# Kernel tuning notes

Measured on AMD Instinct MI355X. Metric: run time of the kernel, lower is better.

The kernel has to match this reference:

```python
import jax, jax.numpy as jnp
import numpy as np

B, N, D_V, D_H, D_K = 1024, 131072, 256, 256, 256


def setup_inputs() -> dict:
    key = jax.random.key(0)
    ks = jax.random.split(key, 12)
    s = 0.02
    V = jax.random.normal(ks[0], (B, D_V), dtype=jnp.float32)
    H = jax.random.normal(ks[1], (N, D_H), dtype=jnp.float32)
    batch_idx = jnp.sort(jax.random.randint(ks[2], (N,), 0, B)).astype(jnp.int32)
    Wq = jax.random.normal(ks[3], (D_K, D_V), dtype=jnp.float32) / np.sqrt(D_V)
    bq = jnp.zeros((D_K,), dtype=jnp.float32)
    Wk = jax.random.normal(ks[4], (D_K, D_H), dtype=jnp.float32) / np.sqrt(D_H)
    bk = jnp.zeros((D_K,), dtype=jnp.float32)
    Wv = jax.random.normal(ks[5], (D_V, D_H), dtype=jnp.float32) / np.sqrt(D_H)
    bv = jnp.zeros((D_V,), dtype=jnp.float32)
    Wo = jax.random.normal(ks[6], (D_V, 2 * D_V), dtype=jnp.float32) / np.sqrt(2 * D_V)
    bo = jnp.zeros((D_V,), dtype=jnp.float32)
    return {"V": V, "H": H, "batch_idx": batch_idx,
            "Wq": Wq, "bq": bq, "Wk": Wk, "bk": bk,
            "Wv": Wv, "bv": bv, "Wo": Wo, "bo": bo}


def reference(V, H, batch_idx, Wq, bq, Wk, bk, Wv, bv, Wo, bo):
    nb = V.shape[0]
    Q = V @ Wq.T + bq            # [B, d_k] one query per graph
    K = H @ Wk.T + bk            # [N, d_k]
    Vval = H @ Wv.T + bv         # [N, d_v]
    scale = 1.0 / jnp.sqrt(jnp.asarray(K.shape[-1], K.dtype))
    # ragged attention scores: each node attends to its graph's query
    scores = jnp.einsum('nd,nd->n', K, Q[batch_idx]) * scale   # [N]
    m = jax.ops.segment_max(scores, batch_idx, num_segments=nb)  # [B]
    e = jnp.exp(scores - m[batch_idx])
    denom = jax.ops.segment_sum(e, batch_idx, num_segments=nb)   # [B]
    attn = e / denom[batch_idx]                                  # [N]
    H_tilde = jax.ops.segment_sum(attn[:, None] * Vval, batch_idx, num_segments=nb)  # [B, d_v]
    U = jnp.concatenate([V, H_tilde], axis=-1)                   # [B, 2*d_v]
    out = U @ Wo.T + bo                                          # [B, d_v]
    # graphs with zero nodes pass V through unchanged
    count = jax.ops.segment_sum(jnp.ones_like(scores), batch_idx, num_segments=nb)
    return jnp.where((count > 0)[:, None], out, V)
```

## Files before the change

### kernel.cpp

```cpp
#include <hip/hip_runtime.h>
#include <math.h>

#define D 256
#define TWOD 512
#define BB 1024
#define NN 131072
#define LOG2E 1.4426950408889634f

typedef float v4f __attribute__((ext_vector_type(4)));

__device__ __forceinline__ v4f ldg_nt(const float* p, bool valid) {
  v4f z = {0.f, 0.f, 0.f, 0.f};
  if (valid) z = __builtin_nontemporal_load((const v4f*)p);
  return z;
}

__device__ __forceinline__ float dot4(v4f a, v4f b) {
  return fmaf(a.w, b.w, fmaf(a.z, b.z, fmaf(a.y, b.y, a.x * b.x)));
}

__global__ __launch_bounds__(256) void prep_kernel(
    const float* __restrict__ Wq, const float* __restrict__ bq,
    const float* __restrict__ Wk, const float* __restrict__ Wv,
    const float* __restrict__ bv, const float* __restrict__ Wo,
    const float* __restrict__ bo, const int* __restrict__ bidx,
    float* __restrict__ Mt, float* __restrict__ WfT,
    float* __restrict__ bqt, float* __restrict__ cvec,
    int* __restrict__ offs) {
  const int blk = blockIdx.x;
  const int t = threadIdx.x;
  if (blk < 64) {
    const int d0 = blk * 4;
    float a0 = 0.f, a1 = 0.f, a2 = 0.f, a3 = 0.f;
    for (int e = 0; e < D; ++e) {
      const float wk = Wk[(size_t)e * D + t];
      const float* wqr = Wq + (size_t)e * D + d0;
      a0 = fmaf(wqr[0], wk, a0);
      a1 = fmaf(wqr[1], wk, a1);
      a2 = fmaf(wqr[2], wk, a2);
      a3 = fmaf(wqr[3], wk, a3);
    }
    Mt[(size_t)(d0 + 0) * D + t] = a0;
    Mt[(size_t)(d0 + 1) * D + t] = a1;
    Mt[(size_t)(d0 + 2) * D + t] = a2;
    Mt[(size_t)(d0 + 3) * D + t] = a3;
  } else if (blk < 128) {
    const int h0 = (blk - 64) * 4;
    float a0 = 0.f, a1 = 0.f, a2 = 0.f, a3 = 0.f;
    for (int v = 0; v < D; ++v) {
      const float wo = Wo[(size_t)t * TWOD + D + v];
      const float* wvr = Wv + (size_t)v * D + h0;
      a0 = fmaf(wvr[0], wo, a0);
      a1 = fmaf(wvr[1], wo, a1);
      a2 = fmaf(wvr[2], wo, a2);
      a3 = fmaf(wvr[3], wo, a3);
    }
    WfT[(size_t)(D + h0 + 0) * D + t] = a0;
    WfT[(size_t)(D + h0 + 1) * D + t] = a1;
    WfT[(size_t)(D + h0 + 2) * D + t] = a2;
    WfT[(size_t)(D + h0 + 3) * D + t] = a3;
  } else if (blk < 144) {
    __shared__ float tile[64][65];
    const int b = blk - 128;
    const int r0 = (b >> 2) * 64, c0 = (b & 3) * 64;
    const int lane = t & 63, sr = t >> 6;
    #pragma unroll 4
    for (int rr = 0; rr < 16; ++rr) {
      const int r = rr * 4 + sr;
      tile[r][lane] = Wo[(size_t)(r0 + r) * TWOD + c0 + lane];
    }
    __syncthreads();
    #pragma unroll 4
    for (int rr = 0; rr < 16; ++rr) {
      const int r = rr * 4 + sr;
      WfT[(size_t)(c0 + r) * D + r0 + lane] = tile[lane][r];
    }
  } else if (blk == 144) {
    float a = 0.f;
    for (int e = 0; e < D; ++e)
      a = fmaf(Wk[(size_t)e * D + t], bq[e], a);
    bqt[t] = a;
  } else if (blk == 145) {
    float a = bo[t];
    for (int v = 0; v < D; ++v)
      a = fmaf(Wo[(size_t)t * TWOD + D + v], bv[v], a);
    cvec[t] = a;
  } else {
    const int i = (blk - 146) * 256 + t;
    if (i >= NN) return;
    const int b1 = bidx[i];
    const int b2 = (i + 1 < NN) ? bidx[i + 1] : BB;
    if (i == 0) {
      for (int b = 0; b <= b1; ++b) offs[b] = 0;
    }
    for (int b = b1 + 1; b <= b2; ++b) offs[b] = i + 1;
  }
}

__global__ __launch_bounds__(1024) void f_kernel(
    const float* __restrict__ H, const float* __restrict__ V,
    const float* __restrict__ Mt, const float* __restrict__ bqt,
    const int* __restrict__ offs, const float* __restrict__ WfT,
    const float* __restrict__ cvec, float* __restrict__ out) {
  __shared__ __align__(16) char smem[32768 + 4096 + 8192];
  float (*partq)[4][D] = (float(*)[4][D])smem;
  float (*ss)[D] = (float(*)[D])smem;
  float (*part)[4][D] = (float(*)[4][D])smem;
  float* Vs  = (float*)(smem + 32768);
  float* Us2 = (float*)(smem + 36864);
  __shared__ float sm[16], sd[16];

  const int t = threadIdx.x;
  const int wave = t >> 6, lane = t & 63;
  const int blk = blockIdx.x;
  const int b0 = blk * 4;

  {
    const int i = t >> 8, d = t & 255;
    Vs[i * 256 + d] = V[(size_t)(b0 + i) * D + d];
  }
  __syncthreads();

  {
    v4f a0 = {0.f, 0.f, 0.f, 0.f}, a1 = a0, a2 = a0, a3 = a0;
    const int db = wave * 16;
    #pragma unroll 4
    for (int dd = 0; dd < 16; ++dd) {
      const int d = db + dd;
      const v4f w4 = *(const v4f*)(Mt + (size_t)d * D + lane * 4);
      a0 += w4 * Vs[0 * 256 + d];
      a1 += w4 * Vs[1 * 256 + d];
      a2 += w4 * Vs[2 * 256 + d];
      a3 += w4 * Vs[3 * 256 + d];
    }
    if (wave >= 8) {
      *(v4f*)&partq[wave - 8][0][lane * 4] = a0;
      *(v4f*)&partq[wave - 8][1][lane * 4] = a1;
      *(v4f*)&partq[wave - 8][2][lane * 4] = a2;
      *(v4f*)&partq[wave - 8][3][lane * 4] = a3;
    }
    __syncthreads();
    if (wave < 8) {
      v4f p0 = *(const v4f*)&partq[wave][0][lane * 4];
      v4f p1 = *(const v4f*)&partq[wave][1][lane * 4];
      v4f p2 = *(const v4f*)&partq[wave][2][lane * 4];
      v4f p3 = *(const v4f*)&partq[wave][3][lane * 4];
      *(v4f*)&partq[wave][0][lane * 4] = a0 + p0;
      *(v4f*)&partq[wave][1][lane * 4] = a1 + p1;
      *(v4f*)&partq[wave][2][lane * 4] = a2 + p2;
      *(v4f*)&partq[wave][3][lane * 4] = a3 + p3;
    }
  }
  __syncthreads();

  const int ib = wave >> 2, qq = wave & 3;
  const int bb = b0 + ib;
  const int start = offs[bb], end = offs[bb + 1];

  v4f q4 = *(const v4f*)(bqt + lane * 4);
  #pragma unroll
  for (int w = 0; w < 8; ++w) q4 += *(const v4f*)&partq[w][ib][lane * 4];
  __syncthreads();

  float m = -1e30f, den = 0.f;
  v4f acc = {0.f, 0.f, 0.f, 0.f};
  {
    const float SC = 0.0625f * LOG2E;
    const int odd = lane & 1;
    int n = start + qq * 2;
    v4f c0 = ldg_nt(H + (size_t)n * D + lane * 4, n < end);
    v4f c1 = ldg_nt(H + (size_t)(n + 1) * D + lane * 4, n + 1 < end);
    while (n < end) {
      const int nn = n + 8;
      v4f p0 = ldg_nt(H + (size_t)nn * D + lane * 4, nn < end);
      v4f p1 = ldg_nt(H + (size_t)(nn + 1) * D + lane * 4, nn + 1 < end);

      const float d0 = dot4(c0, q4);
      const float d1 = dot4(c1, q4);
      const float mine = odd ? d1 : d0;
      const float oth  = odd ? d0 : d1;
      float s = mine + __shfl_xor(oth, 1);
      s += __shfl_xor(s, 2);
      s += __shfl_xor(s, 4);
      s += __shfl_xor(s, 8);
      s += __shfl_xor(s, 16);
      s += __shfl_xor(s, 32);
      const float sc = (n + odd < end) ? s * SC : -1e30f;

      const float mm = fmaxf(sc, __shfl_xor(sc, 1));
      const float nm = fmaxf(m, mm);
      const float f = exp2f(m - nm);
      const float w = exp2f(sc - nm);
      const float wx = __shfl_xor(w, 1);
      const float wr0 = odd ? wx : w;
      const float wr1 = odd ? w : wx;
      den = fmaf(den, f, w + wx);
      acc = acc * f + c0 * wr0 + c1 * wr1;
      m = nm;

      c0 = p0; c1 = p1; n = nn;
    }
  }
  *(v4f*)&ss[wave][lane * 4] = acc;
  if (lane == 0) { sm[wave] = m; sd[wave] = den; }
  __syncthreads();

  {
    const int i = t >> 8, d = t & 255;
    const int w0 = i * 4;
    const float m0 = sm[w0], m1 = sm[w0 + 1], m2 = sm[w0 + 2], m3 = sm[w0 + 3];
    const float M = fmaxf(fmaxf(m0, m1), fmaxf(m2, m3));
    const float f0 = exp2f(m0 - M), f1 = exp2f(m1 - M);
    const float f2 = exp2f(m2 - M), f3 = exp2f(m3 - M);
    const float Dn = sd[w0] * f0 + sd[w0 + 1] * f1 + sd[w0 + 2] * f2 + sd[w0 + 3] * f3;
    const float inv = (Dn > 0.f) ? (1.f / Dn) : 0.f;
    const float sv = (ss[w0][d] * f0 + ss[w0 + 1][d] * f1 +
                      ss[w0 + 2][d] * f2 + ss[w0 + 3][d] * f3) * inv;
    Us2[d * 4 + i] = Vs[i * 256 + d];
    Us2[(D + d) * 4 + i] = sv;
  }
  __syncthreads();

  {
    v4f a0 = {0.f, 0.f, 0.f, 0.f}, a1 = a0, a2 = a0, a3 = a0;
    const int kb = wave * 32;
    #pragma unroll 4
    for (int kk = 0; kk < 32; ++kk) {
      const int k = kb + kk;
      const v4f w4 = *(const v4f*)(WfT + (size_t)k * D + lane * 4);
      const v4f u4 = *(const v4f*)&Us2[k * 4];
      a0 += w4 * u4.x; a1 += w4 * u4.y; a2 += w4 * u4.z; a3 += w4 * u4.w;
    }
    if (wave >= 8) {
      *(v4f*)&part[wave - 8][0][lane * 4] = a0;
      *(v4f*)&part[wave - 8][1][lane * 4] = a1;
      *(v4f*)&part[wave - 8][2][lane * 4] = a2;
      *(v4f*)&part[wave - 8][3][lane * 4] = a3;
    }
    __syncthreads();
    if (wave < 8) {
      v4f p0 = *(const v4f*)&part[wave][0][lane * 4];
      v4f p1 = *(const v4f*)&part[wave][1][lane * 4];
      v4f p2 = *(const v4f*)&part[wave][2][lane * 4];
      v4f p3 = *(const v4f*)&part[wave][3][lane * 4];
      *(v4f*)&part[wave][0][lane * 4] = a0 + p0;
      *(v4f*)&part[wave][1][lane * 4] = a1 + p1;
      *(v4f*)&part[wave][2][lane * 4] = a2 + p2;
      *(v4f*)&part[wave][3][lane * 4] = a3 + p3;
    }
  }
  __syncthreads();
  {
    const int i = t >> 8, d = t & 255;
    const int bb2 = b0 + i;
    float s = cvec[d];
    #pragma unroll
    for (int w = 0; w < 8; ++w) s += part[w][i][d];
    const int c = offs[bb2 + 1] - offs[bb2];
    out[(size_t)bb2 * D + d] = (c > 0) ? s : Us2[d * 4 + i];
  }
}

extern "C" void kernel_launch(void* const* d_in, const int* in_sizes, int n_in,
                              void* d_out, int out_size, void* d_ws, size_t ws_size,
                              hipStream_t stream) {
  const float* V   = (const float*)d_in[0];
  const float* H   = (const float*)d_in[1];
  const int* bidx  = (const int*)d_in[2];
  const float* Wq  = (const float*)d_in[3];
  const float* bq  = (const float*)d_in[4];
  const float* Wk  = (const float*)d_in[5];
  const float* Wv  = (const float*)d_in[7];
  const float* bv  = (const float*)d_in[8];
  const float* Wo  = (const float*)d_in[9];
  const float* bo  = (const float*)d_in[10];
  float* out = (float*)d_out;

  float* ws  = (float*)d_ws;
  float* Mt  = ws;
  float* WfT = Mt + D * D;
  float* bqt = WfT + TWOD * D;
  float* cv  = bqt + D;
  int* offs  = (int*)(cv + D);

  hipLaunchKernelGGL(prep_kernel, dim3(658), dim3(256), 0, stream,
                     Wq, bq, Wk, Wv, bv, Wo, bo, bidx,
                     Mt, WfT, bqt, cv, offs);
  hipLaunchKernelGGL(f_kernel, dim3(BB / 4), dim3(1024), 0, stream,
                     H, V, Mt, bqt, offs, WfT, cv, out);
}
```

Before: 46.25 us.

## Halve graphs per block to two and deepen H prefetch to two stages

Each block of the fused attention kernel now handles 2 graphs with 512 threads instead of 4 graphs with 1024, giving 512 blocks and spreading work across more CUs on the 256-CU part. Shared memory shrinks to match, and the Q projection and output GEMV loops are re-split over 8 waves. The H streaming loop now keeps two iterations of node rows in flight instead of one, to hide more HBM latency. The costs are more blocks each re-reading the Mt and WfT weights, and more registers per thread for the extra prefetch buffers.

```diff
diff --git a/kernel.cpp b/kernel.cpp
--- a/kernel.cpp
+++ b/kernel.cpp
@@ -97,23 +97,23 @@
   }
 }
 
-__global__ __launch_bounds__(1024) void f_kernel(
+__global__ __launch_bounds__(512) void f_kernel(
     const float* __restrict__ H, const float* __restrict__ V,
     const float* __restrict__ Mt, const float* __restrict__ bqt,
     const int* __restrict__ offs, const float* __restrict__ WfT,
     const float* __restrict__ cvec, float* __restrict__ out) {
-  __shared__ __align__(16) char smem[32768 + 4096 + 8192];
-  float (*partq)[4][D] = (float(*)[4][D])smem;
+  __shared__ __align__(16) char smem[8192 + 2048 + 4096];
+  float (*partq)[2][D] = (float(*)[2][D])smem;
   float (*ss)[D] = (float(*)[D])smem;
-  float (*part)[4][D] = (float(*)[4][D])smem;
-  float* Vs  = (float*)(smem + 32768);
-  float* Us2 = (float*)(smem + 36864);
-  __shared__ float sm[16], sd[16];
+  float (*part)[2][D] = (float(*)[2][D])smem;
+  float* Vs  = (float*)(smem + 8192);
+  float* Us2 = (float*)(smem + 10240);
+  __shared__ float sm[8], sd[8];
 
   const int t = threadIdx.x;
   const int wave = t >> 6, lane = t & 63;
   const int blk = blockIdx.x;
-  const int b0 = blk * 4;
+  const int b0 = blk * 2;
 
   {
     const int i = t >> 8, d = t & 255;
@@ -122,33 +122,25 @@
   __syncthreads();
 
   {
-    v4f a0 = {0.f, 0.f, 0.f, 0.f}, a1 = a0, a2 = a0, a3 = a0;
-    const int db = wave * 16;
-    #pragma unroll 4
-    for (int dd = 0; dd < 16; ++dd) {
+    v4f a0 = {0.f, 0.f, 0.f, 0.f}, a1 = a0;
+    const int db = wave * 32;
+    #pragma unroll 4
+    for (int dd = 0; dd < 32; ++dd) {
       const int d = db + dd;
       const v4f w4 = *(const v4f*)(Mt + (size_t)d * D + lane * 4);
       a0 += w4 * Vs[0 * 256 + d];
       a1 += w4 * Vs[1 * 256 + d];
-      a2 += w4 * Vs[2 * 256 + d];
-      a3 += w4 * Vs[3 * 256 + d];
-    }
-    if (wave >= 8) {
-      *(v4f*)&partq[wave - 8][0][lane * 4] = a0;
-      *(v4f*)&partq[wave - 8][1][lane * 4] = a1;
-      *(v4f*)&partq[wave - 8][2][lane * 4] = a2;
-      *(v4f*)&partq[wave - 8][3][lane * 4] = a3;
+    }
+    if (wave >= 4) {
+      *(v4f*)&partq[wave - 4][0][lane * 4] = a0;
+      *(v4f*)&partq[wave - 4][1][lane * 4] = a1;
     }
     __syncthreads();
-    if (wave < 8) {
+    if (wave < 4) {
       v4f p0 = *(const v4f*)&partq[wave][0][lane * 4];
       v4f p1 = *(const v4f*)&partq[wave][1][lane * 4];
-      v4f p2 = *(const v4f*)&partq[wave][2][lane * 4];
-      v4f p3 = *(const v4f*)&partq[wave][3][lane * 4];
       *(v4f*)&partq[wave][0][lane * 4] = a0 + p0;
       *(v4f*)&partq[wave][1][lane * 4] = a1 + p1;
-      *(v4f*)&partq[wave][2][lane * 4] = a2 + p2;
-      *(v4f*)&partq[wave][3][lane * 4] = a3 + p3;
     }
   }
   __syncthreads();
@@ -159,7 +151,7 @@
 
   v4f q4 = *(const v4f*)(bqt + lane * 4);
   #pragma unroll
-  for (int w = 0; w < 8; ++w) q4 += *(const v4f*)&partq[w][ib][lane * 4];
+  for (int w = 0; w < 4; ++w) q4 += *(const v4f*)&partq[w][ib][lane * 4];
   __syncthreads();
 
   float m = -1e30f, den = 0.f;
@@ -170,10 +162,12 @@
     int n = start + qq * 2;
     v4f c0 = ldg_nt(H + (size_t)n * D + lane * 4, n < end);
     v4f c1 = ldg_nt(H + (size_t)(n + 1) * D + lane * 4, n + 1 < end);
+    v4f e0 = ldg_nt(H + (size_t)(n + 8) * D + lane * 4, n + 8 < end);
+    v4f e1 = ldg_nt(H + (size_t)(n + 9) * D + lane * 4, n + 9 < end);
     while (n < end) {
-      const int nn = n + 8;
-      v4f p0 = ldg_nt(H + (size_t)nn * D + lane * 4, nn < end);
-      v4f p1 = ldg_nt(H + (size_t)(nn + 1) * D + lane * 4, nn + 1 < end);
+      const int nf = n + 16;
+      v4f g0 = ldg_nt(H + (size_t)nf * D + lane * 4, nf < end);
+      v4f g1 = ldg_nt(H + (size_t)(nf + 1) * D + lane * 4, nf + 1 < end);
 
       const float d0 = dot4(c0, q4);
       const float d1 = dot4(c1, q4);
@@ -198,7 +192,7 @@
       acc = acc * f + c0 * wr0 + c1 * wr1;
       m = nm;
 
-      c0 = p0; c1 = p1; n = nn;
+      c0 = e0; c1 = e1; e0 = g0; e1 = g1; n += 8;
     }
   }
   *(v4f*)&ss[wave][lane * 4] = acc;
@@ -216,37 +210,32 @@
     const float inv = (Dn > 0.f) ? (1.f / Dn) : 0.f;
     const float sv = (ss[w0][d] * f0 + ss[w0 + 1][d] * f1 +
                       ss[w0 + 2][d] * f2 + ss[w0 + 3][d] * f3) * inv;
-    Us2[d * 4 + i] = Vs[i * 256 + d];
-    Us2[(D + d) * 4 + i] = sv;
-  }
-  __syncthreads();
-
-  {
-    v4f a0 = {0.f, 0.f, 0.f, 0.f}, a1 = a0, a2 = a0, a3 = a0;
-    const int kb = wave * 32;
-    #pragma unroll 4
-    for (int kk = 0; kk < 32; ++kk) {
+    Us2[d * 2 + i] = Vs[i * 256 + d];
+    Us2[(D + d) * 2 + i] = sv;
+  }
+  __syncthreads();
+
+  {
+    v4f a0 = {0.f, 0.f, 0.f, 0.f}, a1 = a0;
+    const int kb = wave * 64;
+    #pragma unroll 4
+    for (int kk = 0; kk < 64; ++kk) {
       const int k = kb + kk;
       const v4f w4 = *(const v4f*)(WfT + (size_t)k * D + lane * 4);
-      const v4f u4 = *(const v4f*)&Us2[k * 4];
-      a0 += w4 * u4.x; a1 += w4 * u4.y; a2 += w4 * u4.z; a3 += w4 * u4.w;
-    }
-    if (wave >= 8) {
-      *(v4f*)&part[wave - 8][0][lane * 4] = a0;
-      *(v4f*)&part[wave - 8][1][lane * 4] = a1;
-      *(v4f*)&part[wave - 8][2][lane * 4] = a2;
-      *(v4f*)&part[wave - 8][3][lane * 4] = a3;
+      const float2 u2 = *(const float2*)&Us2[k * 2];
+      a0 += w4 * u2.x;
+      a1 += w4 * u2.y;
+    }
+    if (wave >= 4) {
+      *(v4f*)&part[wave - 4][0][lane * 4] = a0;
+      *(v4f*)&part[wave - 4][1][lane * 4] = a1;
     }
     __syncthreads();
-    if (wave < 8) {
+    if (wave < 4) {
       v4f p0 = *(const v4f*)&part[wave][0][lane * 4];
       v4f p1 = *(const v4f*)&part[wave][1][lane * 4];
-      v4f p2 = *(const v4f*)&part[wave][2][lane * 4];
-      v4f p3 = *(const v4f*)&part[wave][3][lane * 4];
       *(v4f*)&part[wave][0][lane * 4] = a0 + p0;
       *(v4f*)&part[wave][1][lane * 4] = a1 + p1;
-      *(v4f*)&part[wave][2][lane * 4] = a2 + p2;
-      *(v4f*)&part[wave][3][lane * 4] = a3 + p3;
     }
   }
   __syncthreads();
@@ -255,9 +244,9 @@
     const int bb2 = b0 + i;
     float s = cvec[d];
     #pragma unroll
-    for (int w = 0; w < 8; ++w) s += part[w][i][d];
+    for (int w = 0; w < 4; ++w) s += part[w][i][d];
     const int c = offs[bb2 + 1] - offs[bb2];
-    out[(size_t)bb2 * D + d] = (c > 0) ? s : Us2[d * 4 + i];
+    out[(size_t)bb2 * D + d] = (c > 0) ? s : Vs[i * 256 + d];
   }
 }
 
@@ -286,6 +275,6 @@
   hipLaunchKernelGGL(prep_kernel, dim3(658), dim3(256), 0, stream,
                      Wq, bq, Wk, Wv, bv, Wo, bo, bidx,
                      Mt, WfT, bqt, cv, offs);
-  hipLaunchKernelGGL(f_kernel, dim3(BB / 4), dim3(1024), 0, stream,
+  hipLaunchKernelGGL(f_kernel, dim3(BB / 2), dim3(512), 0, stream,
                      H, V, Mt, bqt, offs, WfT, cv, out);
 }
```

Result: slower. 50.60 us (+9.4%).

## Balance waves across graphs by node count and prefetch H before Q projection

Applied to the files above, without the earlier changes.

Each block's 16 waves are now split among its 4 graphs in proportion to each graph's node count (largest remainder), so graphs with more nodes get more waves instead of a fixed 4 each. The first H rows are loaded before the Q-projection phase so their memory latency overlaps that compute. The prep kernel's Mt computation now uses vectorized loads across 4 wave groups with a shared-memory reduction. This adds a serial thread-0 allocation step and variable-length merge loops.

```diff
diff --git a/kernel.cpp b/kernel.cpp
--- a/kernel.cpp
+++ b/kernel.cpp
@@ -30,20 +30,28 @@
   const int blk = blockIdx.x;
   const int t = threadIdx.x;
   if (blk < 64) {
+    __shared__ __align__(16) float part[4][4][D];
+    const int wq = t >> 6, lane = t & 63;
     const int d0 = blk * 4;
-    float a0 = 0.f, a1 = 0.f, a2 = 0.f, a3 = 0.f;
-    for (int e = 0; e < D; ++e) {
-      const float wk = Wk[(size_t)e * D + t];
+    v4f a0 = {0.f, 0.f, 0.f, 0.f}, a1 = a0, a2 = a0, a3 = a0;
+    for (int ee = 0; ee < 64; ++ee) {
+      const int e = wq * 64 + ee;
+      const v4f wk4 = *(const v4f*)&Wk[(size_t)e * D + lane * 4];
       const float* wqr = Wq + (size_t)e * D + d0;
-      a0 = fmaf(wqr[0], wk, a0);
-      a1 = fmaf(wqr[1], wk, a1);
-      a2 = fmaf(wqr[2], wk, a2);
-      a3 = fmaf(wqr[3], wk, a3);
-    }
-    Mt[(size_t)(d0 + 0) * D + t] = a0;
-    Mt[(size_t)(d0 + 1) * D + t] = a1;
-    Mt[(size_t)(d0 + 2) * D + t] = a2;
-    Mt[(size_t)(d0 + 3) * D + t] = a3;
+      a0 += wk4 * wqr[0];
+      a1 += wk4 * wqr[1];
+      a2 += wk4 * wqr[2];
+      a3 += wk4 * wqr[3];
+    }
+    *(v4f*)&part[wq][0][lane * 4] = a0;
+    *(v4f*)&part[wq][1][lane * 4] = a1;
+    *(v4f*)&part[wq][2][lane * 4] = a2;
+    *(v4f*)&part[wq][3][lane * 4] = a3;
+    __syncthreads();
+    #pragma unroll
+    for (int r = 0; r < 4; ++r)
+      Mt[(size_t)(d0 + r) * D + t] =
+          part[0][r][t] + part[1][r][t] + part[2][r][t] + part[3][r][t];
   } else if (blk < 128) {
     const int h0 = (blk - 64) * 4;
     float a0 = 0.f, a1 = 0.f, a2 = 0.f, a3 = 0.f;
@@ -109,6 +117,8 @@
   float* Vs  = (float*)(smem + 32768);
   float* Us2 = (float*)(smem + 36864);
   __shared__ float sm[16], sd[16];
+  __shared__ int soff[5];
+  __shared__ int wpre[5];
 
   const int t = threadIdx.x;
   const int wave = t >> 6, lane = t & 63;
@@ -119,7 +129,64 @@
     const int i = t >> 8, d = t & 255;
     Vs[i * 256 + d] = V[(size_t)(b0 + i) * D + d];
   }
-  __syncthreads();
+  if (t == 0) {
+    int c[4], C = 0, ne = 0;
+    #pragma unroll
+    for (int i = 0; i < 4; ++i) {
+      soff[i] = offs[b0 + i];
+    }
+    soff[4] = offs[b0 + 4];
+    #pragma unroll
+    for (int i = 0; i < 4; ++i) {
+      c[i] = soff[i + 1] - soff[i];
+      C += c[i];
+      if (c[i] > 0) ne++;
+    }
+    int w[4] = {0, 0, 0, 0};
+    if (C > 0) {
+      const int R = 16 - ne;
+      long rem[4];
+      int sumex = 0;
+      #pragma unroll
+      for (int i = 0; i < 4; ++i) {
+        if (c[i] > 0) {
+          const long num = (long)R * c[i];
+          const int ex = (int)(num / C);
+          w[i] = 1 + ex;
+          rem[i] = num - (long)ex * C;
+          sumex += ex;
+        } else {
+          rem[i] = -1;
+        }
+      }
+      int L = R - sumex;
+      while (L > 0) {
+        int arg = 0;
+        long best = -2;
+        #pragma unroll
+        for (int i = 0; i < 4; ++i)
+          if (rem[i] > best) { best = rem[i]; arg = i; }
+        w[arg] += 1;
+        rem[arg] = -2;
+        --L;
+      }
+    }
+    wpre[0] = 0;
+    #pragma unroll
+    for (int i = 0; i < 4; ++i) wpre[i + 1] = wpre[i] + w[i];
+  }
+  __syncthreads();
+
+  int myi = -1, ph = 0, nw = 1;
+  #pragma unroll
+  for (int i = 0; i < 4; ++i)
+    if (wave >= wpre[i] && wave < wpre[i + 1]) { myi = i; ph = wave - wpre[i]; nw = wpre[i + 1] - wpre[i]; }
+  const int start = (myi >= 0) ? soff[myi] : 0;
+  const int end   = (myi >= 0) ? soff[myi + 1] : 0;
+  const int S2 = 2 * nw;
+  int n = start + ph * 2;
+  v4f c0 = ldg_nt(H + (size_t)n * D + lane * 4, n < end);
+  v4f c1 = ldg_nt(H + (size_t)(n + 1) * D + lane * 4, n + 1 < end);
 
   {
     v4f a0 = {0.f, 0.f, 0.f, 0.f}, a1 = a0, a2 = a0, a3 = a0;
@@ -153,13 +220,10 @@
   }
   __syncthreads();
 
-  const int ib = wave >> 2, qq = wave & 3;
-  const int bb = b0 + ib;
-  const int start = offs[bb], end = offs[bb + 1];
-
+  const int qb = (myi >= 0) ? myi : 0;
   v4f q4 = *(const v4f*)(bqt + lane * 4);
   #pragma unroll
-  for (int w = 0; w < 8; ++w) q4 += *(const v4f*)&partq[w][ib][lane * 4];
+  for (int w = 0; w < 8; ++w) q4 += *(const v4f*)&partq[w][qb][lane * 4];
   __syncthreads();
 
   float m = -1e30f, den = 0.f;
@@ -167,11 +231,8 @@
   {
     const float SC = 0.0625f * LOG2E;
     const int odd = lane & 1;
-    int n = start + qq * 2;
-    v4f c0 = ldg_nt(H + (size_t)n * D + lane * 4, n < end);
-    v4f c1 = ldg_nt(H + (size_t)(n + 1) * D + lane * 4, n + 1 < end);
     while (n < end) {
-      const int nn = n + 8;
+      const int nn = n + S2;
       v4f p0 = ldg_nt(H + (size_t)nn * D + lane * 4, nn < end);
       v4f p1 = ldg_nt(H + (size_t)(nn + 1) * D + lane * 4, nn + 1 < end);
 
@@ -207,17 +268,18 @@
 
   {
     const int i = t >> 8, d = t & 255;
-    const int w0 = i * 4;
-    const float m0 = sm[w0], m1 = sm[w0 + 1], m2 = sm[w0 + 2], m3 = sm[w0 + 3];
-    const float M = fmaxf(fmaxf(m0, m1), fmaxf(m2, m3));
-    const float f0 = exp2f(m0 - M), f1 = exp2f(m1 - M);
-    const float f2 = exp2f(m2 - M), f3 = exp2f(m3 - M);
-    const float Dn = sd[w0] * f0 + sd[w0 + 1] * f1 + sd[w0 + 2] * f2 + sd[w0 + 3] * f3;
+    const int W0 = wpre[i], W1 = wpre[i + 1];
+    float M = -1e30f;
+    for (int w = W0; w < W1; ++w) M = fmaxf(M, sm[w]);
+    float Dn = 0.f, sv = 0.f;
+    for (int w = W0; w < W1; ++w) {
+      const float f = exp2f(sm[w] - M);
+      Dn = fmaf(sd[w], f, Dn);
+      sv = fmaf(ss[w][d], f, sv);
+    }
     const float inv = (Dn > 0.f) ? (1.f / Dn) : 0.f;
-    const float sv = (ss[w0][d] * f0 + ss[w0 + 1][d] * f1 +
-                      ss[w0 + 2][d] * f2 + ss[w0 + 3][d] * f3) * inv;
     Us2[d * 4 + i] = Vs[i * 256 + d];
-    Us2[(D + d) * 4 + i] = sv;
+    Us2[(D + d) * 4 + i] = sv * inv;
   }
   __syncthreads();
 
@@ -256,7 +318,7 @@
     float s = cvec[d];
     #pragma unroll
     for (int w = 0; w < 8; ++w) s += part[w][i][d];
-    const int c = offs[bb2 + 1] - offs[bb2];
+    const int c = soff[i + 1] - soff[i];
     out[(size_t)bb2 * D + d] = (c > 0) ? s : Us2[d * 4 + i];
   }
 }
```

Result: no change. 46.66 us (+0.9%).

## Issue H prefetch before query projection, use contiguous per-wave chunks, split prep reduction

Applied to the files above, without the earlier changes.

The main kernel now loads segment offsets into shared memory and issues the first four H row loads before the query-projection GEMV, so the HBM latency of the attention stream overlaps that compute. Each wave now walks a contiguous quarter of its graph's nodes with a two-deep prefetch, instead of strided interleaved pairs. In the prep kernel the Wq·Wk product is split across four waves along the reduction dimension using vector loads and a shared-memory reduction, which shortens the serial 256-step loop. In exchange the prefetched rows keep more registers live across the GEMV phase, and the prep kernel uses extra shared memory.

```diff
diff --git a/kernel.cpp b/kernel.cpp
--- a/kernel.cpp
+++ b/kernel.cpp
@@ -30,20 +30,28 @@
   const int blk = blockIdx.x;
   const int t = threadIdx.x;
   if (blk < 64) {
+    __shared__ __align__(16) float part[4][4][D];
+    const int wq = t >> 6, lane = t & 63;
     const int d0 = blk * 4;
-    float a0 = 0.f, a1 = 0.f, a2 = 0.f, a3 = 0.f;
-    for (int e = 0; e < D; ++e) {
-      const float wk = Wk[(size_t)e * D + t];
+    v4f a0 = {0.f, 0.f, 0.f, 0.f}, a1 = a0, a2 = a0, a3 = a0;
+    for (int ee = 0; ee < 64; ++ee) {
+      const int e = wq * 64 + ee;
+      const v4f wk4 = *(const v4f*)&Wk[(size_t)e * D + lane * 4];
       const float* wqr = Wq + (size_t)e * D + d0;
-      a0 = fmaf(wqr[0], wk, a0);
-      a1 = fmaf(wqr[1], wk, a1);
-      a2 = fmaf(wqr[2], wk, a2);
-      a3 = fmaf(wqr[3], wk, a3);
-    }
-    Mt[(size_t)(d0 + 0) * D + t] = a0;
-    Mt[(size_t)(d0 + 1) * D + t] = a1;
-    Mt[(size_t)(d0 + 2) * D + t] = a2;
-    Mt[(size_t)(d0 + 3) * D + t] = a3;
+      a0 += wk4 * wqr[0];
+      a1 += wk4 * wqr[1];
+      a2 += wk4 * wqr[2];
+      a3 += wk4 * wqr[3];
+    }
+    *(v4f*)&part[wq][0][lane * 4] = a0;
+    *(v4f*)&part[wq][1][lane * 4] = a1;
+    *(v4f*)&part[wq][2][lane * 4] = a2;
+    *(v4f*)&part[wq][3][lane * 4] = a3;
+    __syncthreads();
+    #pragma unroll
+    for (int r = 0; r < 4; ++r)
+      Mt[(size_t)(d0 + r) * D + t] =
+          part[0][r][t] + part[1][r][t] + part[2][r][t] + part[3][r][t];
   } else if (blk < 128) {
     const int h0 = (blk - 64) * 4;
     float a0 = 0.f, a1 = 0.f, a2 = 0.f, a3 = 0.f;
@@ -109,17 +117,31 @@
   float* Vs  = (float*)(smem + 32768);
   float* Us2 = (float*)(smem + 36864);
   __shared__ float sm[16], sd[16];
+  __shared__ int soff[5];
 
   const int t = threadIdx.x;
   const int wave = t >> 6, lane = t & 63;
   const int blk = blockIdx.x;
   const int b0 = blk * 4;
 
+  if (t < 5) soff[t] = offs[b0 + t];
   {
     const int i = t >> 8, d = t & 255;
     Vs[i * 256 + d] = V[(size_t)(b0 + i) * D + d];
   }
   __syncthreads();
+
+  const int ib = wave >> 2, ph = wave & 3;
+  const int start = soff[ib];
+  const int cnt = soff[ib + 1] - start;
+  const int ck = (cnt + 3) >> 2;
+  const int s0 = start + min(cnt, ph * ck);
+  const int e0 = start + min(cnt, (ph + 1) * ck);
+  int n = s0;
+  v4f c0 = ldg_nt(H + (size_t)n * D + lane * 4, n < e0);
+  v4f c1 = ldg_nt(H + (size_t)(n + 1) * D + lane * 4, n + 1 < e0);
+  v4f f0 = ldg_nt(H + (size_t)(n + 2) * D + lane * 4, n + 2 < e0);
+  v4f f1 = ldg_nt(H + (size_t)(n + 3) * D + lane * 4, n + 3 < e0);
 
   {
     v4f a0 = {0.f, 0.f, 0.f, 0.f}, a1 = a0, a2 = a0, a3 = a0;
@@ -153,10 +175,6 @@
   }
   __syncthreads();
 
-  const int ib = wave >> 2, qq = wave & 3;
-  const int bb = b0 + ib;
-  const int start = offs[bb], end = offs[bb + 1];
-
   v4f q4 = *(const v4f*)(bqt + lane * 4);
   #pragma unroll
   for (int w = 0; w < 8; ++w) q4 += *(const v4f*)&partq[w][ib][lane * 4];
@@ -167,13 +185,10 @@
   {
     const float SC = 0.0625f * LOG2E;
     const int odd = lane & 1;
-    int n = start + qq * 2;
-    v4f c0 = ldg_nt(H + (size_t)n * D + lane * 4, n < end);
-    v4f c1 = ldg_nt(H + (size_t)(n + 1) * D + lane * 4, n + 1 < end);
-    while (n < end) {
-      const int nn = n + 8;
-      v4f p0 = ldg_nt(H + (size_t)nn * D + lane * 4, nn < end);
-      v4f p1 = ldg_nt(H + (size_t)(nn + 1) * D + lane * 4, nn + 1 < end);
+    while (n < e0) {
+      const int nn = n + 4;
+      v4f g0 = ldg_nt(H + (size_t)nn * D + lane * 4, nn < e0);
+      v4f g1 = ldg_nt(H + (size_t)(nn + 1) * D + lane * 4, nn + 1 < e0);
 
       const float d0 = dot4(c0, q4);
       const float d1 = dot4(c1, q4);
@@ -185,7 +200,7 @@
       s += __shfl_xor(s, 8);
       s += __shfl_xor(s, 16);
       s += __shfl_xor(s, 32);
-      const float sc = (n + odd < end) ? s * SC : -1e30f;
+      const float sc = (n + odd < e0) ? s * SC : -1e30f;
 
       const float mm = fmaxf(sc, __shfl_xor(sc, 1));
       const float nm = fmaxf(m, mm);
@@ -198,7 +213,7 @@
       acc = acc * f + c0 * wr0 + c1 * wr1;
       m = nm;
 
-      c0 = p0; c1 = p1; n = nn;
+      c0 = f0; c1 = f1; f0 = g0; f1 = g1; n += 2;
     }
   }
   *(v4f*)&ss[wave][lane * 4] = acc;
@@ -210,12 +225,12 @@
     const int w0 = i * 4;
     const float m0 = sm[w0], m1 = sm[w0 + 1], m2 = sm[w0 + 2], m3 = sm[w0 + 3];
     const float M = fmaxf(fmaxf(m0, m1), fmaxf(m2, m3));
-    const float f0 = exp2f(m0 - M), f1 = exp2f(m1 - M);
-    const float f2 = exp2f(m2 - M), f3 = exp2f(m3 - M);
-    const float Dn = sd[w0] * f0 + sd[w0 + 1] * f1 + sd[w0 + 2] * f2 + sd[w0 + 3] * f3;
+    const float f0m = exp2f(m0 - M), f1m = exp2f(m1 - M);
+    const float f2m = exp2f(m2 - M), f3m = exp2f(m3 - M);
+    const float Dn = sd[w0] * f0m + sd[w0 + 1] * f1m + sd[w0 + 2] * f2m + sd[w0 + 3] * f3m;
     const float inv = (Dn > 0.f) ? (1.f / Dn) : 0.f;
-    const float sv = (ss[w0][d] * f0 + ss[w0 + 1][d] * f1 +
-                      ss[w0 + 2][d] * f2 + ss[w0 + 3][d] * f3) * inv;
+    const float sv = (ss[w0][d] * f0m + ss[w0 + 1][d] * f1m +
+                      ss[w0 + 2][d] * f2m + ss[w0 + 3][d] * f3m) * inv;
     Us2[d * 4 + i] = Vs[i * 256 + d];
     Us2[(D + d) * 4 + i] = sv;
   }
@@ -256,7 +271,7 @@
     float s = cvec[d];
     #pragma unroll
     for (int w = 0; w < 8; ++w) s += part[w][i][d];
-    const int c = offs[bb2 + 1] - offs[bb2];
+    const int c = soff[i + 1] - soff[i];
     out[(size_t)bb2 * D + d] = (c > 0) ? s : Us2[d * 4 + i];
   }
 }
```

New measurement: 46.79 us. Within noise of the previous version (+1.2%).
